# Performance work log

Measured on AMD Instinct MI355X. Metric: run time of the kernel, lower is better.

## Reference

```python
import jax, jax.numpy as jnp
import numpy as np

B, T, D = 4, 4096, 512
H, L = 8, 6
HD = D // H
BS = 64          # block_size
MLP = 2048
VOCAB = 96000
MAX_SCALE = 10000.0
LN_EPS = 1e-6


def _sinusoidal_pe(length, dim, max_scale=MAX_SCALE):
    # flax common_layers sinusoidal init (concat sin|cos halves)
    pos = np.arange(length)[:, None].astype(np.float32)
    div = np.exp(np.arange(0, dim, 2).astype(np.float32) * -(np.log(max_scale) / dim))
    pe = np.zeros((length, dim), dtype=np.float32)
    pe[:, : dim // 2] = np.sin(pos * div)
    pe[:, dim // 2:] = np.cos(pos * div)
    return jnp.asarray(pe)

_PE = _sinusoidal_pe(T, D)


def layer_norm(x, scale, bias):
    m = jnp.mean(x, axis=-1, keepdims=True)
    v = jnp.mean(jnp.square(x - m), axis=-1, keepdims=True)
    return (x - m) * jax.lax.rsqrt(v + LN_EPS) * scale + bias


def local_block_attention(x, mask, wq, wk, wv, wo, stagger):
    # x: [B, T, D], mask: [B, T] bool (True = real token)
    b, t, d = x.shape
    if stagger:
        lp = BS // 2
        rp = BS - lp
        x = jnp.pad(x, ((0, 0), (lp, rp), (0, 0)))
        mask = jnp.pad(mask, ((0, 0), (lp, rp)))
    tp = x.shape[1]
    nb = tp // BS
    xb = x.reshape(b, nb, BS, d)          # [B, nb, BS, D]
    mb = mask.reshape(b, nb, BS)          # [B, nb, BS]
    scale = 1.0 / float(np.sqrt(HD))
    q = jnp.einsum('bnsd,dhf->bnshf', xb, wq) * scale
    k = jnp.einsum('bnsd,dhf->bnshf', xb, wk)
    v = jnp.einsum('bnsd,dhf->bnshf', xb, wv)
    scores = jnp.einsum('bnqhf,bnkhf->bnhqk', q, k)       # [B, nb, H, BS, BS]
    scores = jnp.where(mb[:, :, None, None, :], scores, jnp.asarray(-1e9, scores.dtype))
    probs = jax.nn.softmax(scores, axis=-1)
    o = jnp.einsum('bnhqk,bnkhf->bnqhf', probs, v)
    o = jnp.einsum('bnqhf,hfd->bnqd', o, wo).reshape(b, tp, d)
    if stagger:
        o = o[:, lp:lp + t]
    return o


def setup_inputs() -> dict:
    key = jax.random.key(0)
    ks = jax.random.split(key, 10)
    inputs = jax.random.randint(ks[0], (B, T), 0, VOCAB)
    embed = jax.random.normal(ks[1], (VOCAB, D), dtype=jnp.float32)
    s = 0.02
    wq = jax.random.normal(ks[2], (L, D, H, HD), dtype=jnp.float32) * s
    wk = jax.random.normal(ks[3], (L, D, H, HD), dtype=jnp.float32) * s
    wv = jax.random.normal(ks[4], (L, D, H, HD), dtype=jnp.float32) * s
    wo = jax.random.normal(ks[5], (L, H, HD, D), dtype=jnp.float32) * s
    w1 = jax.random.normal(ks[6], (L, D, MLP), dtype=jnp.float32) * s
    b1 = jnp.zeros((L, MLP), dtype=jnp.float32)
    w2 = jax.random.normal(ks[7], (L, MLP, D), dtype=jnp.float32) * s
    b2 = jnp.zeros((L, D), dtype=jnp.float32)
    ln1_s = jnp.ones((L, D), dtype=jnp.float32)
    ln1_b = jnp.zeros((L, D), dtype=jnp.float32)
    ln2_s = jnp.ones((L, D), dtype=jnp.float32)
    ln2_b = jnp.zeros((L, D), dtype=jnp.float32)
    lnf_s = jnp.ones((D,), dtype=jnp.float32)
    lnf_b = jnp.zeros((D,), dtype=jnp.float32)
    return {'inputs': inputs, 'embed': embed, 'wq': wq, 'wk': wk, 'wv': wv, 'wo': wo,
            'ln1_s': ln1_s, 'ln1_b': ln1_b, 'ln2_s': ln2_s, 'ln2_b': ln2_b,
            'w1': w1, 'b1': b1, 'w2': w2, 'b2': b2, 'lnf_s': lnf_s, 'lnf_b': lnf_b}


def reference(inputs, embed, wq, wk, wv, wo, ln1_s, ln1_b, ln2_s, ln2_b,
              w1, b1, w2, b2, lnf_s, lnf_b):
    mask = inputs > 0                      # src padding mask [B, T]
    x = embed[inputs.astype(jnp.int32)]    # [B, T, D]
    x = x + _PE[None, :, :]                # sinusoidal position embedding
    for lyr in range(L):
        stagger = (lyr % 2 == 1)           # stagger_local_blocks on odd layers
        h = layer_norm(x, ln1_s[lyr], ln1_b[lyr])
        h = local_block_attention(h, mask, wq[lyr], wk[lyr], wv[lyr], wo[lyr], stagger)
        x = x + h
        y = layer_norm(x, ln2_s[lyr], ln2_b[lyr])
        y = jnp.matmul(jax.nn.relu(jnp.matmul(y, w1[lyr]) + b1[lyr]), w2[lyr]) + b2[lyr]
        x = x + y
    return layer_norm(x, lnf_s, lnf_b)
```

## Files before the change

kernel.cpp:

```cpp
#include <hip/hip_runtime.h>

typedef unsigned short u16;
typedef unsigned int   u32;
typedef __attribute__((ext_vector_type(8))) short short8;
typedef __attribute__((ext_vector_type(4))) float f32x4;

#define TSEQ   4096
#define DMODEL 512
#define NHEAD  8
#define HDIM   64
#define NLAYER 6
#define MLPD   2048

#define GPTR(p) (const __attribute__((address_space(1))) void*)(p)
#define LPTR(p) (__attribute__((address_space(3))) void*)(p)

__device__ __forceinline__ u16 f2b(float f) {
  u32 u = __float_as_uint(f);
  u32 r = (u + 0x7fffu + ((u >> 16) & 1u)) >> 16;
  return (u16)r;
}
__device__ __forceinline__ float b2f(u16 h) { return __uint_as_float(((u32)h) << 16); }
__device__ __forceinline__ float bflo(u32 u) { return __uint_as_float(u << 16); }
__device__ __forceinline__ float bfhi(u32 u) { return __uint_as_float(u & 0xffff0000u); }

__device__ __forceinline__ void unp8(uint4 u, float* d) {
  d[0] = bflo(u.x); d[1] = bfhi(u.x);
  d[2] = bflo(u.y); d[3] = bfhi(u.y);
  d[4] = bflo(u.z); d[5] = bfhi(u.z);
  d[6] = bflo(u.w); d[7] = bfhi(u.w);
}

__global__ __launch_bounds__(256) void transpose_convert(
    const float* __restrict__ W, u16* __restrict__ out,
    int K, int N, int Ntot, int ro) {
  __shared__ float tile[64][65];
  int l  = blockIdx.z;
  int k0 = blockIdx.x * 64, n0 = blockIdx.y * 64;
  const float* Wl = W + (size_t)l * K * N;
  u16* Ol = out + (size_t)l * Ntot * K;
  int tx = threadIdx.x & 15, ty = threadIdx.x >> 4;
#pragma unroll
  for (int p = 0; p < 4; ++p) {
    int k = k0 + p * 16 + ty;
    float4 v = *(const float4*)(Wl + (size_t)k * N + n0 + tx * 4);
    tile[p * 16 + ty][tx * 4 + 0] = v.x;
    tile[p * 16 + ty][tx * 4 + 1] = v.y;
    tile[p * 16 + ty][tx * 4 + 2] = v.z;
    tile[p * 16 + ty][tx * 4 + 3] = v.w;
  }
  __syncthreads();
#pragma unroll
  for (int p = 0; p < 4; ++p) {
    int n = n0 + p * 16 + ty;
    ushort4 s;
    s.x = f2b(tile[tx * 4 + 0][p * 16 + ty]);
    s.y = f2b(tile[tx * 4 + 1][p * 16 + ty]);
    s.z = f2b(tile[tx * 4 + 2][p * 16 + ty]);
    s.w = f2b(tile[tx * 4 + 3][p * 16 + ty]);
    *(ushort4*)(Ol + (size_t)(ro + n) * K + k0 + tx * 4) = s;
  }
}

__global__ void embed_pe_kernel(const int* __restrict__ idx,
                                const float* __restrict__ embed,
                                float* __restrict__ x) {
  int i = blockIdx.x;
  int t = i & (TSEQ - 1);
  int tok = idx[i];
  int c = threadIdx.x * 4;
  float4 e = *(const float4*)(embed + (size_t)tok * DMODEL + c);
  float vals[4] = {e.x, e.y, e.z, e.w};
  float o[4];
#pragma unroll
  for (int j = 0; j < 4; ++j) {
    int col = c + j;
    int jj = (col < 256) ? col : col - 256;
    float div = __expf((float)jj * -0.035977892078032f);
    float arg = (float)t * div;
    o[j] = vals[j] + ((col < 256) ? __sinf(arg) : __cosf(arg));
  }
  float4 r = {o[0], o[1], o[2], o[3]};
  *(float4*)(x + (size_t)i * DMODEL + c) = r;
}

template <bool OUT_BF16>
__global__ __launch_bounds__(256) void ln_kernel(
    const float* __restrict__ x, const float* __restrict__ gamma,
    const float* __restrict__ beta, void* __restrict__ out) {
  int wave = threadIdx.x >> 6, lane = threadIdx.x & 63;
  int row = (blockIdx.x << 2) + wave;
  const float* xr = x + (size_t)row * DMODEL + lane * 8;
  float4 a = *(const float4*)xr;
  float4 b = *(const float4*)(xr + 4);
  float v[8] = {a.x, a.y, a.z, a.w, b.x, b.y, b.z, b.w};
  float s = 0.f;
#pragma unroll
  for (int j = 0; j < 8; ++j) s += v[j];
#pragma unroll
  for (int off = 1; off < 64; off <<= 1) s += __shfl_xor(s, off, 64);
  float mean = s * (1.0f / 512.0f);
  float q = 0.f;
#pragma unroll
  for (int j = 0; j < 8; ++j) { float d = v[j] - mean; q += d * d; }
#pragma unroll
  for (int off = 1; off < 64; off <<= 1) q += __shfl_xor(q, off, 64);
  float rstd = rsqrtf(q * (1.0f / 512.0f) + 1e-6f);
  float4 g0 = *(const float4*)(gamma + lane * 8);
  float4 g1 = *(const float4*)(gamma + lane * 8 + 4);
  float4 p0 = *(const float4*)(beta + lane * 8);
  float4 p1 = *(const float4*)(beta + lane * 8 + 4);
  float g[8] = {g0.x, g0.y, g0.z, g0.w, g1.x, g1.y, g1.z, g1.w};
  float be[8] = {p0.x, p0.y, p0.z, p0.w, p1.x, p1.y, p1.z, p1.w};
  float r[8];
#pragma unroll
  for (int j = 0; j < 8; ++j) r[j] = (v[j] - mean) * rstd * g[j] + be[j];
  if (OUT_BF16) {
    uint4 pk;
    pk.x = (u32)f2b(r[0]) | ((u32)f2b(r[1]) << 16);
    pk.y = (u32)f2b(r[2]) | ((u32)f2b(r[3]) << 16);
    pk.z = (u32)f2b(r[4]) | ((u32)f2b(r[5]) << 16);
    pk.w = (u32)f2b(r[6]) | ((u32)f2b(r[7]) << 16);
    *(uint4*)((u16*)out + (size_t)row * DMODEL + lane * 8) = pk;
  } else {
    float4 r0 = {r[0], r[1], r[2], r[3]};
    float4 r1 = {r[4], r[5], r[6], r[7]};
    float* op = (float*)out + (size_t)row * DMODEL + lane * 8;
    *(float4*)op = r0;
    *(float4*)(op + 4) = r1;
  }
}

template <int FLAGS>
__global__ __launch_bounds__(256) void gemm_kernel(
    const u16* __restrict__ A, const u16* __restrict__ Bt,
    const float* __restrict__ bias, const float* __restrict__ resid,
    void* __restrict__ out, int M, int N, int K) {
  __shared__ __align__(16) u16 a_lds[128][32];
  __shared__ __align__(16) u16 b_lds[128][32];
  int m0 = blockIdx.y * 128, n0 = blockIdx.x * 128;
  int t = threadIdx.x;
  int lr = t >> 2, lc = (t & 3) * 8;
  int wave = t >> 6, lane = t & 63;
  int wm = (wave >> 1) * 64, wn = (wave & 1) * 64;
  int fr = lane & 15, quad = lane >> 4;

  f32x4 acc[4][4];
  f32x4 zz = {0.f, 0.f, 0.f, 0.f};
#pragma unroll
  for (int i = 0; i < 4; ++i)
#pragma unroll
    for (int j = 0; j < 4; ++j) acc[i][j] = zz;

  const u16* Ag0 = A + (size_t)(m0 + lr) * K + lc;
  const u16* Ag1 = A + (size_t)(m0 + lr + 64) * K + lc;
  const u16* Bg0 = Bt + (size_t)(n0 + lr) * K + lc;
  const u16* Bg1 = Bt + (size_t)(n0 + lr + 64) * K + lc;
  u16* lA0 = &a_lds[lr][lc];
  u16* lA1 = &a_lds[lr + 64][lc];
  u16* lB0 = &b_lds[lr][lc];
  u16* lB1 = &b_lds[lr + 64][lc];

  for (int k0 = 0; k0 < K; k0 += 32) {
    __syncthreads();
    __builtin_amdgcn_global_load_lds(GPTR(Ag0 + k0), LPTR(lA0), 16, 0, 0);
    __builtin_amdgcn_global_load_lds(GPTR(Ag1 + k0), LPTR(lA1), 16, 0, 0);
    __builtin_amdgcn_global_load_lds(GPTR(Bg0 + k0), LPTR(lB0), 16, 0, 0);
    __builtin_amdgcn_global_load_lds(GPTR(Bg1 + k0), LPTR(lB1), 16, 0, 0);
    __syncthreads();
    short8 af[4], bf[4];
#pragma unroll
    for (int mi = 0; mi < 4; ++mi)
      af[mi] = *(const short8*)&a_lds[wm + mi * 16 + fr][quad * 8];
#pragma unroll
    for (int ni = 0; ni < 4; ++ni)
      bf[ni] = *(const short8*)&b_lds[wn + ni * 16 + fr][quad * 8];
#pragma unroll
    for (int mi = 0; mi < 4; ++mi)
#pragma unroll
      for (int ni = 0; ni < 4; ++ni)
        acc[mi][ni] = __builtin_amdgcn_mfma_f32_16x16x32_bf16(
            af[mi], bf[ni], acc[mi][ni], 0, 0, 0);
  }

#pragma unroll
  for (int mi = 0; mi < 4; ++mi)
#pragma unroll
    for (int ni = 0; ni < 4; ++ni) {
      int colg = n0 + wn + ni * 16 + fr;
      float bv = (FLAGS & 1) ? bias[colg] : 0.0f;
#pragma unroll
      for (int r = 0; r < 4; ++r) {
        int rowg = m0 + wm + mi * 16 + quad * 4 + r;
        float val = acc[mi][ni][r] + bv;
        if (FLAGS & 2) val = fmaxf(val, 0.0f);
        if (FLAGS & 4) val += resid[(size_t)rowg * N + colg];
        if (FLAGS & 8)
          ((u16*)out)[(size_t)rowg * N + colg] = f2b(val);
        else
          ((float*)out)[(size_t)rowg * N + colg] = val;
      }
    }
}

__global__ __launch_bounds__(256) void attn_kernel(
    const u16* __restrict__ qkv, const int* __restrict__ tokens,
    u16* __restrict__ o, int sh) {
  __shared__ __align__(16) float qs[64][68];
  __shared__ __align__(16) float ks[64][68];
  __shared__ __align__(16) u16 vs[64][64];
  __shared__ __align__(16) float ss[64][65];
  __shared__ float kmask[64];
  int n = blockIdx.x, h = blockIdx.y, b = blockIdx.z;
  int tid = threadIdx.x;
  {
    int srow = tid >> 2;
    int cg = (tid & 3) << 4;
    int p = n * 64 + srow - sh;
    if (tid < 64) {
      int pp = n * 64 + tid - sh;
      kmask[tid] =
          (pp >= 0 && pp < TSEQ && tokens[(size_t)b * TSEQ + pp] > 0) ? 1.0f : 0.0f;
    }
    if (p >= 0 && p < TSEQ) {
      const u16* base = qkv + ((size_t)(b * TSEQ + p)) * 1536 + h * HDIM + cg;
      uint4 qa = *(const uint4*)(base);
      uint4 qb = *(const uint4*)(base + 8);
      uint4 ka = *(const uint4*)(base + 512);
      uint4 kb = *(const uint4*)(base + 520);
      uint4 va = *(const uint4*)(base + 1024);
      uint4 vb = *(const uint4*)(base + 1032);
      unp8(qa, &qs[srow][cg]);
      unp8(qb, &qs[srow][cg + 8]);
      unp8(ka, &ks[srow][cg]);
      unp8(kb, &ks[srow][cg + 8]);
      *(uint4*)&vs[srow][cg] = va;
      *(uint4*)&vs[srow][cg + 8] = vb;
    } else {
      float4 z4 = {0.f, 0.f, 0.f, 0.f};
      uint4 z = {0u, 0u, 0u, 0u};
#pragma unroll
      for (int j = 0; j < 4; ++j) {
        *(float4*)&qs[srow][cg + 4 * j] = z4;
        *(float4*)&ks[srow][cg + 4 * j] = z4;
      }
      *(uint4*)&vs[srow][cg] = z;
      *(uint4*)&vs[srow][cg + 8] = z;
    }
  }
  __syncthreads();
  int i0 = (tid >> 4) << 2;
  int c0 = (tid & 15) << 2;
  float a4[4][4];
#pragma unroll
  for (int a = 0; a < 4; ++a)
#pragma unroll
    for (int c = 0; c < 4; ++c) a4[a][c] = 0.f;
  for (int f = 0; f < 64; f += 4) {
    float4 qv[4], kv[4];
#pragma unroll
    for (int a = 0; a < 4; ++a) qv[a] = *(const float4*)&qs[i0 + a][f];
#pragma unroll
    for (int c = 0; c < 4; ++c) kv[c] = *(const float4*)&ks[c0 + c][f];
#pragma unroll
    for (int a = 0; a < 4; ++a)
#pragma unroll
      for (int c = 0; c < 4; ++c)
        a4[a][c] += qv[a].x * kv[c].x + qv[a].y * kv[c].y +
                    qv[a].z * kv[c].z + qv[a].w * kv[c].w;
  }
#pragma unroll
  for (int a = 0; a < 4; ++a)
#pragma unroll
    for (int c = 0; c < 4; ++c)
      ss[i0 + a][c0 + c] =
          (kmask[c0 + c] > 0.f) ? 0.125f * a4[a][c] : -1.0e9f;
  __syncthreads();
  if (tid < 64) {
    float m = -3.0e38f;
#pragma unroll
    for (int j = 0; j < 64; ++j) m = fmaxf(m, ss[tid][j]);
    float sum = 0.f;
#pragma unroll
    for (int j = 0; j < 64; ++j) {
      float e = __expf(ss[tid][j] - m);
      ss[tid][j] = e;
      sum += e;
    }
    float inv = 1.0f / sum;
#pragma unroll
    for (int j = 0; j < 64; ++j) ss[tid][j] *= inv;
  }
  __syncthreads();
  float o4[4][4];
#pragma unroll
  for (int a = 0; a < 4; ++a)
#pragma unroll
    for (int c = 0; c < 4; ++c) o4[a][c] = 0.f;
  for (int j = 0; j < 64; ++j) {
    float pv[4];
#pragma unroll
    for (int a = 0; a < 4; ++a) pv[a] = ss[i0 + a][j];
    ushort4 vraw = *(const ushort4*)&vs[j][c0];
    float v0 = b2f(vraw.x), v1 = b2f(vraw.y), v2 = b2f(vraw.z), v3 = b2f(vraw.w);
#pragma unroll
    for (int a = 0; a < 4; ++a) {
      o4[a][0] += pv[a] * v0;
      o4[a][1] += pv[a] * v1;
      o4[a][2] += pv[a] * v2;
      o4[a][3] += pv[a] * v3;
    }
  }
#pragma unroll
  for (int a = 0; a < 4; ++a) {
    int pq = n * 64 + i0 + a - sh;
    if (pq >= 0 && pq < TSEQ) {
      ushort4 st;
      st.x = f2b(o4[a][0]);
      st.y = f2b(o4[a][1]);
      st.z = f2b(o4[a][2]);
      st.w = f2b(o4[a][3]);
      *(ushort4*)(o + ((size_t)(b * TSEQ + pq)) * DMODEL + h * HDIM + c0) = st;
    }
  }
}

extern "C" void kernel_launch(void* const* d_in, const int* in_sizes, int n_in,
                              void* d_out, int out_size, void* d_ws, size_t ws_size,
                              hipStream_t stream) {
  (void)in_sizes; (void)n_in; (void)out_size; (void)ws_size;
  const int*   tokens = (const int*)d_in[0];
  const float* embed  = (const float*)d_in[1];
  const float* wq = (const float*)d_in[2];
  const float* wk = (const float*)d_in[3];
  const float* wv = (const float*)d_in[4];
  const float* wo = (const float*)d_in[5];
  const float* ln1_s = (const float*)d_in[6];
  const float* ln1_b = (const float*)d_in[7];
  const float* ln2_s = (const float*)d_in[8];
  const float* ln2_b = (const float*)d_in[9];
  const float* w1 = (const float*)d_in[10];
  const float* b1 = (const float*)d_in[11];
  const float* w2 = (const float*)d_in[12];
  const float* b2 = (const float*)d_in[13];
  const float* lnf_s = (const float*)d_in[14];
  const float* lnf_b = (const float*)d_in[15];

  char* ws = (char*)d_ws;
  const size_t MB = 1024ull * 1024ull;
  float* x     = (float*)(ws + 0);
  u16* h       = (u16*)(ws + 32 * MB);
  u16* qkv     = (u16*)(ws + 48 * MB);
  u16* obuf    = (u16*)(ws + 96 * MB);
  u16* hidden  = (u16*)(ws + 48 * MB);
  u16* wqkv_bt = (u16*)(ws + 112 * MB);
  u16* wo_bt   = (u16*)(ws + 121 * MB);
  u16* w1_bt   = (u16*)(ws + 124 * MB);
  u16* w2_bt   = (u16*)(ws + 136 * MB);

  transpose_convert<<<dim3(8, 8, 6), 256, 0, stream>>>(wq, wqkv_bt, 512, 512, 1536, 0);
  transpose_convert<<<dim3(8, 8, 6), 256, 0, stream>>>(wk, wqkv_bt, 512, 512, 1536, 512);
  transpose_convert<<<dim3(8, 8, 6), 256, 0, stream>>>(wv, wqkv_bt, 512, 512, 1536, 1024);
  transpose_convert<<<dim3(8, 8, 6), 256, 0, stream>>>(wo, wo_bt, 512, 512, 512, 0);
  transpose_convert<<<dim3(8, 32, 6), 256, 0, stream>>>(w1, w1_bt, 512, 2048, 2048, 0);
  transpose_convert<<<dim3(32, 8, 6), 256, 0, stream>>>(w2, w2_bt, 2048, 512, 512, 0);

  embed_pe_kernel<<<16384, 128, 0, stream>>>(tokens, embed, x);

  for (int l = 0; l < NLAYER; ++l) {
    int sh = (l & 1) ? 32 : 0;
    int nb = (l & 1) ? 65 : 64;
    ln_kernel<true><<<4096, 256, 0, stream>>>(x, ln1_s + l * 512, ln1_b + l * 512, h);
    gemm_kernel<8><<<dim3(12, 128), 256, 0, stream>>>(
        h, wqkv_bt + (size_t)l * 1536 * 512, nullptr, nullptr, qkv, 16384, 1536, 512);
    attn_kernel<<<dim3(nb, NHEAD, 4), 256, 0, stream>>>(qkv, tokens, obuf, sh);
    gemm_kernel<4><<<dim3(4, 128), 256, 0, stream>>>(
        obuf, wo_bt + (size_t)l * 512 * 512, nullptr, x, x, 16384, 512, 512);
    ln_kernel<true><<<4096, 256, 0, stream>>>(x, ln2_s + l * 512, ln2_b + l * 512, h);
    gemm_kernel<1 | 2 | 8><<<dim3(16, 128), 256, 0, stream>>>(
        h, w1_bt + (size_t)l * 2048 * 512, b1 + l * 2048, nullptr, hidden, 16384, 2048, 512);
    gemm_kernel<1 | 4><<<dim3(4, 128), 256, 0, stream>>>(
        hidden, w2_bt + (size_t)l * 512 * 2048, b2 + l * 512, x, x, 16384, 512, 2048);
  }
  ln_kernel<false><<<4096, 256, 0, stream>>>(x, lnf_s, lnf_b, d_out);
}
```

Before: 1.826 ms.

## Rewrite block attention with MFMA and emit transposed V from QKV GEMM

After: 1.628 ms. 10.8% less time.

```diff
diff --git a/kernel.cpp b/kernel.cpp
--- a/kernel.cpp
+++ b/kernel.cpp
@@ -21,22 +21,39 @@
   return (u16)r;
 }
 __device__ __forceinline__ float b2f(u16 h) { return __uint_as_float(((u32)h) << 16); }
-__device__ __forceinline__ float bflo(u32 u) { return __uint_as_float(u << 16); }
-__device__ __forceinline__ float bfhi(u32 u) { return __uint_as_float(u & 0xffff0000u); }
-
-__device__ __forceinline__ void unp8(uint4 u, float* d) {
-  d[0] = bflo(u.x); d[1] = bfhi(u.x);
-  d[2] = bflo(u.y); d[3] = bfhi(u.y);
-  d[4] = bflo(u.z); d[5] = bfhi(u.z);
-  d[6] = bflo(u.w); d[7] = bfhi(u.w);
-}
-
-__global__ __launch_bounds__(256) void transpose_convert(
-    const float* __restrict__ W, u16* __restrict__ out,
-    int K, int N, int Ntot, int ro) {
+
+__device__ __forceinline__ short8 ld8g(const u16* p, bool ok) {
+  if (ok) return *(const short8*)p;
+  short8 z = {0, 0, 0, 0, 0, 0, 0, 0};
+  return z;
+}
+
+__global__ __launch_bounds__(256) void transpose_convert_all(
+    const float* __restrict__ wq, const float* __restrict__ wk,
+    const float* __restrict__ wv, const float* __restrict__ wo,
+    const float* __restrict__ w1, const float* __restrict__ w2,
+    u16* __restrict__ wqkv_bt, u16* __restrict__ wo_bt,
+    u16* __restrict__ w1_bt, u16* __restrict__ w2_bt) {
   __shared__ float tile[64][65];
-  int l  = blockIdx.z;
-  int k0 = blockIdx.x * 64, n0 = blockIdx.y * 64;
+  int bx = blockIdx.x, l = blockIdx.y;
+  const float* W; u16* out; int K, N, Ntot, ro, kb, nb2;
+  if (bx < 256) {
+    int which = bx >> 6, local = bx & 63;
+    K = 512; N = 512; kb = local & 7; nb2 = local >> 3;
+    if (which == 0)      { W = wq; out = wqkv_bt; Ntot = 1536; ro = 0; }
+    else if (which == 1) { W = wk; out = wqkv_bt; Ntot = 1536; ro = 512; }
+    else if (which == 2) { W = wv; out = wqkv_bt; Ntot = 1536; ro = 1024; }
+    else                 { W = wo; out = wo_bt;   Ntot = 512;  ro = 0; }
+  } else if (bx < 512) {
+    int local = bx - 256;
+    W = w1; out = w1_bt; K = 512; N = 2048; Ntot = 2048; ro = 0;
+    kb = local & 7; nb2 = local >> 3;
+  } else {
+    int local = bx - 512;
+    W = w2; out = w2_bt; K = 2048; N = 512; Ntot = 512; ro = 0;
+    kb = local >> 3; nb2 = local & 7;
+  }
+  int k0 = kb * 64, n0 = nb2 * 64;
   const float* Wl = W + (size_t)l * K * N;
   u16* Ol = out + (size_t)l * Ntot * K;
   int tx = threadIdx.x & 15, ty = threadIdx.x >> 4;
@@ -135,7 +152,7 @@
 __global__ __launch_bounds__(256) void gemm_kernel(
     const u16* __restrict__ A, const u16* __restrict__ Bt,
     const float* __restrict__ bias, const float* __restrict__ resid,
-    void* __restrict__ out, int M, int N, int K) {
+    void* __restrict__ out, void* __restrict__ out2, int M, int N, int K) {
   __shared__ __align__(16) u16 a_lds[128][32];
   __shared__ __align__(16) u16 b_lds[128][32];
   int m0 = blockIdx.y * 128, n0 = blockIdx.x * 128;
@@ -181,6 +198,34 @@
       for (int ni = 0; ni < 4; ++ni)
         acc[mi][ni] = __builtin_amdgcn_mfma_f32_16x16x32_bf16(
             af[mi], bf[ni], acc[mi][ni], 0, 0, 0);
+  }
+
+  if (FLAGS & 16) {
+#pragma unroll
+    for (int mi = 0; mi < 4; ++mi)
+#pragma unroll
+      for (int ni = 0; ni < 4; ++ni) {
+        int colg = n0 + wn + ni * 16 + fr;
+        if (colg < 1024) {
+#pragma unroll
+          for (int r = 0; r < 4; ++r) {
+            int rowg = m0 + wm + mi * 16 + quad * 4 + r;
+            ((u16*)out)[(size_t)rowg * 1024 + colg] = f2b(acc[mi][ni][r]);
+          }
+        } else {
+          int hh = (colg - 1024) >> 6, ff = colg & 63;
+          int rowg0 = m0 + wm + mi * 16 + quad * 4;
+          int bb = rowg0 >> 12, tok = rowg0 & 4095;
+          ushort4 pk;
+          pk.x = f2b(acc[mi][ni][0]);
+          pk.y = f2b(acc[mi][ni][1]);
+          pk.z = f2b(acc[mi][ni][2]);
+          pk.w = f2b(acc[mi][ni][3]);
+          *(ushort4*)((u16*)out2 +
+                      ((size_t)(bb * 8 + hh) * 64 + ff) * 4096 + tok) = pk;
+        }
+      }
+    return;
   }
 
 #pragma unroll
@@ -203,126 +248,139 @@
     }
 }
 
-__global__ __launch_bounds__(256) void attn_kernel(
-    const u16* __restrict__ qkv, const int* __restrict__ tokens,
-    u16* __restrict__ o, int sh) {
-  __shared__ __align__(16) float qs[64][68];
-  __shared__ __align__(16) float ks[64][68];
-  __shared__ __align__(16) u16 vs[64][64];
-  __shared__ __align__(16) float ss[64][65];
+__global__ __launch_bounds__(128) void attn_mfma_kernel(
+    const u16* __restrict__ qk, const u16* __restrict__ vt,
+    const int* __restrict__ tokens, u16* __restrict__ o, int sh) {
+  __shared__ __align__(16) u16 ps[2][64][72];
   __shared__ float kmask[64];
-  int n = blockIdx.x, h = blockIdx.y, b = blockIdx.z;
+  int n = blockIdx.x, hg = blockIdx.y, b = blockIdx.z;
   int tid = threadIdx.x;
-  {
-    int srow = tid >> 2;
-    int cg = (tid & 3) << 4;
-    int p = n * 64 + srow - sh;
-    if (tid < 64) {
-      int pp = n * 64 + tid - sh;
-      kmask[tid] =
-          (pp >= 0 && pp < TSEQ && tokens[(size_t)b * TSEQ + pp] > 0) ? 1.0f : 0.0f;
+  int w = tid >> 6, lane = tid & 63;
+  int head = hg * 2 + w;
+  int fr = lane & 15, quad = lane >> 4;
+
+  if (tid < 64) {
+    int pp = n * 64 + tid - sh;
+    kmask[tid] =
+        (pp >= 0 && pp < TSEQ && tokens[(size_t)b * TSEQ + pp] > 0) ? 1.f : 0.f;
+  }
+  __syncthreads();
+
+  const u16* qkb = qk + (size_t)b * TSEQ * 1024;
+
+  f32x4 st[4][4];
+  f32x4 zz = {0.f, 0.f, 0.f, 0.f};
+#pragma unroll
+  for (int i = 0; i < 4; ++i)
+#pragma unroll
+    for (int j = 0; j < 4; ++j) st[i][j] = zz;
+#pragma unroll
+  for (int kk = 0; kk < 2; ++kk) {
+    short8 ka[4], qb[4];
+#pragma unroll
+    for (int mi = 0; mi < 4; ++mi) {
+      int p = n * 64 + mi * 16 + fr - sh;
+      ka[mi] = ld8g(qkb + (ptrdiff_t)p * 1024 + 512 + head * 64 + kk * 32 + quad * 8,
+                    p >= 0 && p < TSEQ);
     }
-    if (p >= 0 && p < TSEQ) {
-      const u16* base = qkv + ((size_t)(b * TSEQ + p)) * 1536 + h * HDIM + cg;
-      uint4 qa = *(const uint4*)(base);
-      uint4 qb = *(const uint4*)(base + 8);
-      uint4 ka = *(const uint4*)(base + 512);
-      uint4 kb = *(const uint4*)(base + 520);
-      uint4 va = *(const uint4*)(base + 1024);
-      uint4 vb = *(const uint4*)(base + 1032);
-      unp8(qa, &qs[srow][cg]);
-      unp8(qb, &qs[srow][cg + 8]);
-      unp8(ka, &ks[srow][cg]);
-      unp8(kb, &ks[srow][cg + 8]);
-      *(uint4*)&vs[srow][cg] = va;
-      *(uint4*)&vs[srow][cg + 8] = vb;
-    } else {
-      float4 z4 = {0.f, 0.f, 0.f, 0.f};
-      uint4 z = {0u, 0u, 0u, 0u};
-#pragma unroll
-      for (int j = 0; j < 4; ++j) {
-        *(float4*)&qs[srow][cg + 4 * j] = z4;
-        *(float4*)&ks[srow][cg + 4 * j] = z4;
+#pragma unroll
+    for (int ni = 0; ni < 4; ++ni) {
+      int p = n * 64 + ni * 16 + fr - sh;
+      qb[ni] = ld8g(qkb + (ptrdiff_t)p * 1024 + head * 64 + kk * 32 + quad * 8,
+                    p >= 0 && p < TSEQ);
+    }
+#pragma unroll
+    for (int mi = 0; mi < 4; ++mi)
+#pragma unroll
+      for (int ni = 0; ni < 4; ++ni)
+        st[mi][ni] = __builtin_amdgcn_mfma_f32_16x16x32_bf16(
+            ka[mi], qb[ni], st[mi][ni], 0, 0, 0);
+  }
+
+  float kmv[4][4];
+#pragma unroll
+  for (int mi = 0; mi < 4; ++mi)
+#pragma unroll
+    for (int r = 0; r < 4; ++r) kmv[mi][r] = kmask[mi * 16 + quad * 4 + r];
+#pragma unroll
+  for (int ni = 0; ni < 4; ++ni) {
+    float mx = -3.0e38f;
+#pragma unroll
+    for (int mi = 0; mi < 4; ++mi)
+#pragma unroll
+      for (int r = 0; r < 4; ++r) {
+        float s = (kmv[mi][r] > 0.f) ? st[mi][ni][r] * 0.125f : -1.0e9f;
+        st[mi][ni][r] = s;
+        mx = fmaxf(mx, s);
       }
-      *(uint4*)&vs[srow][cg] = z;
-      *(uint4*)&vs[srow][cg + 8] = z;
+    mx = fmaxf(mx, __shfl_xor(mx, 16, 64));
+    mx = fmaxf(mx, __shfl_xor(mx, 32, 64));
+    float sm = 0.f;
+#pragma unroll
+    for (int mi = 0; mi < 4; ++mi)
+#pragma unroll
+      for (int r = 0; r < 4; ++r) {
+        float e = __expf(st[mi][ni][r] - mx);
+        st[mi][ni][r] = e;
+        sm += e;
+      }
+    sm += __shfl_xor(sm, 16, 64);
+    sm += __shfl_xor(sm, 32, 64);
+    float inv = 1.0f / sm;
+#pragma unroll
+    for (int mi = 0; mi < 4; ++mi)
+#pragma unroll
+      for (int r = 0; r < 4; ++r) st[mi][ni][r] *= inv;
+  }
+
+#pragma unroll
+  for (int mi = 0; mi < 4; ++mi)
+#pragma unroll
+    for (int ni = 0; ni < 4; ++ni) {
+      uint2 pk;
+      pk.x = (u32)f2b(st[mi][ni][0]) | ((u32)f2b(st[mi][ni][1]) << 16);
+      pk.y = (u32)f2b(st[mi][ni][2]) | ((u32)f2b(st[mi][ni][3]) << 16);
+      *(uint2*)&ps[w][ni * 16 + fr][mi * 16 + quad * 4] = pk;
     }
-  }
   __syncthreads();
-  int i0 = (tid >> 4) << 2;
-  int c0 = (tid & 15) << 2;
-  float a4[4][4];
-#pragma unroll
-  for (int a = 0; a < 4; ++a)
-#pragma unroll
-    for (int c = 0; c < 4; ++c) a4[a][c] = 0.f;
-  for (int f = 0; f < 64; f += 4) {
-    float4 qv[4], kv[4];
-#pragma unroll
-    for (int a = 0; a < 4; ++a) qv[a] = *(const float4*)&qs[i0 + a][f];
-#pragma unroll
-    for (int c = 0; c < 4; ++c) kv[c] = *(const float4*)&ks[c0 + c][f];
-#pragma unroll
-    for (int a = 0; a < 4; ++a)
-#pragma unroll
-      for (int c = 0; c < 4; ++c)
-        a4[a][c] += qv[a].x * kv[c].x + qv[a].y * kv[c].y +
-                    qv[a].z * kv[c].z + qv[a].w * kv[c].w;
-  }
-#pragma unroll
-  for (int a = 0; a < 4; ++a)
-#pragma unroll
-    for (int c = 0; c < 4; ++c)
-      ss[i0 + a][c0 + c] =
-          (kmask[c0 + c] > 0.f) ? 0.125f * a4[a][c] : -1.0e9f;
-  __syncthreads();
-  if (tid < 64) {
-    float m = -3.0e38f;
-#pragma unroll
-    for (int j = 0; j < 64; ++j) m = fmaxf(m, ss[tid][j]);
-    float sum = 0.f;
-#pragma unroll
-    for (int j = 0; j < 64; ++j) {
-      float e = __expf(ss[tid][j] - m);
-      ss[tid][j] = e;
-      sum += e;
-    }
-    float inv = 1.0f / sum;
-#pragma unroll
-    for (int j = 0; j < 64; ++j) ss[tid][j] *= inv;
-  }
-  __syncthreads();
-  float o4[4][4];
-#pragma unroll
-  for (int a = 0; a < 4; ++a)
-#pragma unroll
-    for (int c = 0; c < 4; ++c) o4[a][c] = 0.f;
-  for (int j = 0; j < 64; ++j) {
-    float pv[4];
-#pragma unroll
-    for (int a = 0; a < 4; ++a) pv[a] = ss[i0 + a][j];
-    ushort4 vraw = *(const ushort4*)&vs[j][c0];
-    float v0 = b2f(vraw.x), v1 = b2f(vraw.y), v2 = b2f(vraw.z), v3 = b2f(vraw.w);
-#pragma unroll
-    for (int a = 0; a < 4; ++a) {
-      o4[a][0] += pv[a] * v0;
-      o4[a][1] += pv[a] * v1;
-      o4[a][2] += pv[a] * v2;
-      o4[a][3] += pv[a] * v3;
-    }
-  }
-#pragma unroll
-  for (int a = 0; a < 4; ++a) {
-    int pq = n * 64 + i0 + a - sh;
-    if (pq >= 0 && pq < TSEQ) {
-      ushort4 st;
-      st.x = f2b(o4[a][0]);
-      st.y = f2b(o4[a][1]);
-      st.z = f2b(o4[a][2]);
-      st.w = f2b(o4[a][3]);
-      *(ushort4*)(o + ((size_t)(b * TSEQ + pq)) * DMODEL + h * HDIM + c0) = st;
-    }
-  }
+
+  f32x4 oc[4][4];
+#pragma unroll
+  for (int i = 0; i < 4; ++i)
+#pragma unroll
+    for (int j = 0; j < 4; ++j) oc[i][j] = zz;
+  const u16* vtb = vt + (size_t)(b * 8 + head) * 64 * 4096;
+#pragma unroll
+  for (int kk = 0; kk < 2; ++kk) {
+    short8 pa[4], vb[4];
+#pragma unroll
+    for (int mi = 0; mi < 4; ++mi)
+      pa[mi] = *(const short8*)&ps[w][mi * 16 + fr][kk * 32 + quad * 8];
+    int key0 = n * 64 - sh + kk * 32 + quad * 8;
+    bool kok = (key0 >= 0) && (key0 < TSEQ);
+#pragma unroll
+    for (int ni = 0; ni < 4; ++ni)
+      vb[ni] = ld8g(vtb + (size_t)(ni * 16 + fr) * 4096 + key0, kok);
+#pragma unroll
+    for (int mi = 0; mi < 4; ++mi)
+#pragma unroll
+      for (int ni = 0; ni < 4; ++ni)
+        oc[mi][ni] = __builtin_amdgcn_mfma_f32_16x16x32_bf16(
+            pa[mi], vb[ni], oc[mi][ni], 0, 0, 0);
+  }
+
+#pragma unroll
+  for (int mi = 0; mi < 4; ++mi)
+#pragma unroll
+    for (int ni = 0; ni < 4; ++ni)
+#pragma unroll
+      for (int r = 0; r < 4; ++r) {
+        int q = mi * 16 + quad * 4 + r;
+        int p = n * 64 + q - sh;
+        if (p >= 0 && p < TSEQ)
+          o[((size_t)(b * TSEQ + p)) * DMODEL + head * 64 + ni * 16 + fr] =
+              f2b(oc[mi][ni][r]);
+      }
 }
 
 extern "C" void kernel_launch(void* const* d_in, const int* in_sizes, int n_in,
@@ -350,20 +408,17 @@
   const size_t MB = 1024ull * 1024ull;
   float* x     = (float*)(ws + 0);
   u16* h       = (u16*)(ws + 32 * MB);
-  u16* qkv     = (u16*)(ws + 48 * MB);
-  u16* obuf    = (u16*)(ws + 96 * MB);
+  u16* qk      = (u16*)(ws + 48 * MB);
+  u16* vt      = (u16*)(ws + 82 * MB);
+  u16* obuf    = (u16*)(ws + 99 * MB);
   u16* hidden  = (u16*)(ws + 48 * MB);
-  u16* wqkv_bt = (u16*)(ws + 112 * MB);
-  u16* wo_bt   = (u16*)(ws + 121 * MB);
-  u16* w1_bt   = (u16*)(ws + 124 * MB);
-  u16* w2_bt   = (u16*)(ws + 136 * MB);
-
-  transpose_convert<<<dim3(8, 8, 6), 256, 0, stream>>>(wq, wqkv_bt, 512, 512, 1536, 0);
-  transpose_convert<<<dim3(8, 8, 6), 256, 0, stream>>>(wk, wqkv_bt, 512, 512, 1536, 512);
-  transpose_convert<<<dim3(8, 8, 6), 256, 0, stream>>>(wv, wqkv_bt, 512, 512, 1536, 1024);
-  transpose_convert<<<dim3(8, 8, 6), 256, 0, stream>>>(wo, wo_bt, 512, 512, 512, 0);
-  transpose_convert<<<dim3(8, 32, 6), 256, 0, stream>>>(w1, w1_bt, 512, 2048, 2048, 0);
-  transpose_convert<<<dim3(32, 8, 6), 256, 0, stream>>>(w2, w2_bt, 2048, 512, 512, 0);
+  u16* wqkv_bt = (u16*)(ws + 116 * MB);
+  u16* wo_bt   = (u16*)(ws + 126 * MB);
+  u16* w1_bt   = (u16*)(ws + 130 * MB);
+  u16* w2_bt   = (u16*)(ws + 143 * MB);
+
+  transpose_convert_all<<<dim3(768, 6), 256, 0, stream>>>(
+      wq, wk, wv, wo, w1, w2, wqkv_bt, wo_bt, w1_bt, w2_bt);
 
   embed_pe_kernel<<<16384, 128, 0, stream>>>(tokens, embed, x);
 
@@ -371,16 +426,20 @@
     int sh = (l & 1) ? 32 : 0;
     int nb = (l & 1) ? 65 : 64;
     ln_kernel<true><<<4096, 256, 0, stream>>>(x, ln1_s + l * 512, ln1_b + l * 512, h);
-    gemm_kernel<8><<<dim3(12, 128), 256, 0, stream>>>(
-        h, wqkv_bt + (size_t)l * 1536 * 512, nullptr, nullptr, qkv, 16384, 1536, 512);
-    attn_kernel<<<dim3(nb, NHEAD, 4), 256, 0, stream>>>(qkv, tokens, obuf, sh);
+    gemm_kernel<16><<<dim3(12, 128), 256, 0, stream>>>(
+        h, wqkv_bt + (size_t)l * 1536 * 512, nullptr, nullptr, qk, vt,
+        16384, 1536, 512);
+    attn_mfma_kernel<<<dim3(nb, 4, 4), 128, 0, stream>>>(qk, vt, tokens, obuf, sh);
     gemm_kernel<4><<<dim3(4, 128), 256, 0, stream>>>(
-        obuf, wo_bt + (size_t)l * 512 * 512, nullptr, x, x, 16384, 512, 512);
+        obuf, wo_bt + (size_t)l * 512 * 512, nullptr, x, x, nullptr,
+        16384, 512, 512);
     ln_kernel<true><<<4096, 256, 0, stream>>>(x, ln2_s + l * 512, ln2_b + l * 512, h);
     gemm_kernel<1 | 2 | 8><<<dim3(16, 128), 256, 0, stream>>>(
-        h, w1_bt + (size_t)l * 2048 * 512, b1 + l * 2048, nullptr, hidden, 16384, 2048, 512);
+        h, w1_bt + (size_t)l * 2048 * 512, b1 + l * 2048, nullptr, hidden, nullptr,
+        16384, 2048, 512);
     gemm_kernel<1 | 4><<<dim3(4, 128), 256, 0, stream>>>(
-        hidden, w2_bt + (size_t)l * 512 * 2048, b2 + l * 512, x, x, 16384, 512, 2048);
+        hidden, w2_bt + (size_t)l * 512 * 2048, b2 + l * 512, x, x, nullptr,
+        16384, 512, 2048);
   }
   ln_kernel<false><<<4096, 256, 0, stream>>>(x, lnf_s, lnf_b, d_out);
 }
```
